# Kernel tuning notes

Hardware: AMD Instinct MI355X
Metric: run time of the kernel (lower is better)

Reference implementation:

```python
import jax, jax.numpy as jnp
import numpy as np

N, E, F, B = 50000, 100000, 80000, 64   # nodes, edges, faces, graphs
S, T, D = 32, 32, 3                      # bump_steps, num_thetas, num_features
R = 1.1
SHARP = 500.0                            # sigmoid sharpness from the source


def setup_inputs() -> dict:
    key = jax.random.key(0)
    k = jax.random.split(key, 6)
    x = jax.random.normal(k[0], (N, D), dtype=jnp.float32)
    node_weights = jax.random.uniform(k[1], (N,), dtype=jnp.float32)
    v = jax.random.uniform(k[2], (D, T), dtype=jnp.float32) - 0.5  # Parameter init: rand - 0.5
    lin = jnp.linspace(-R, R, S).astype(jnp.float32)               # bump thresholds
    edge_index = jax.random.randint(k[3], (2, E), 0, N)
    face = jax.random.randint(k[4], (3, F), 0, N)
    batch = jnp.sort(jax.random.randint(k[5], (N,), 0, B))         # sorted graph ids per node
    return {"x": x, "node_weights": node_weights, "v": v, "lin": lin,
            "edge_index": edge_index, "face": face, "batch": batch}


def _wecc(h, index, lin, weight):
    # h: [M, T] heights, index: [M] graph ids, weight: [M]
    # ecc: [M, S, T] = sigmoid(500*(lin - h)) * weight, then scatter-add by graph.
    ecc = jax.nn.sigmoid(SHARP * (lin[None, :, None] - h[:, None, :])) * weight[:, None, None]
    # segment_sum over simplices == index_add on dim 1 followed by movedim(0,1) -> [B, S, T]
    return jax.ops.segment_sum(ecc, index, num_segments=B)


def reference(x, node_weights, v, lin, edge_index, face, batch):
    nh = x @ v                                   # [N, T] node heights
    eh = jnp.min(nh[edge_index], axis=0)         # [E, T] edge height = min of endpoints
    fh = jnp.min(nh[face], axis=0)               # [F, T] face height = min of vertices
    edge_w = jnp.max(node_weights[edge_index], axis=0)  # [E]
    face_w = jnp.max(node_weights[face], axis=0)        # [F]
    out = _wecc(nh, batch, lin, node_weights)
    out = out - _wecc(eh, batch[edge_index[0]], lin, edge_w)
    out = out + _wecc(fh, batch[face[0]], lin, face_w)
    return out  # [B, S, T]
```

## Files before the change

### kernel.cpp

```cpp
#include <hip/hip_runtime.h>

#define NB      64
#define SS      32
#define TT      32
#define RADIUSF 1.1f
#define NC      16
#define NROWS   34
#define NCNT    128
#define BCAP    1440

__global__ __launch_bounds__(256) void k_pre(
    const int* __restrict__ ei, const int* __restrict__ fc,
    const int* __restrict__ batch,
    int* __restrict__ cntp, int* __restrict__ cur, int* __restrict__ ns,
    int Nn, int E, int F)
{
    const int tid = threadIdx.x;
    if ((int)blockIdx.x < NCNT) {
        __shared__ int lc[NB];
        const int blk = blockIdx.x;
        const int EF = E + F;
        if (tid < NB) lc[tid] = 0;
        __syncthreads();
        const int j0 = (int)((long long)EF * blk / NCNT);
        const int j1 = (int)((long long)EF * (blk + 1) / NCNT);
        for (int j = j0 + tid; j < j1; j += 256) {
            const int i0 = (j < E) ? ei[j] : fc[j - E];
            atomicAdd(&lc[batch[i0]], 1);
        }
        __syncthreads();
        if (tid < NB) cntp[blk * NB + tid] = lc[tid];
    } else {
        if (tid < NB) cur[tid] = 0;
        if (tid <= NB) {
            int lo = 0, hi = Nn;
            while (lo < hi) { const int mid = (lo + hi) >> 1; if (batch[mid] < tid) lo = mid + 1; else hi = mid; }
            ns[tid] = lo;
        }
    }
}

__global__ __launch_bounds__(256) void k_build(
    const float* __restrict__ nw, const int* __restrict__ ei,
    const int* __restrict__ fc, const int* __restrict__ batch,
    const int* __restrict__ cntp, int* __restrict__ cur,
    int* __restrict__ ebase_g, int4* __restrict__ U, int E, int F)
{
    __shared__ int s_sum[4][NB];
    __shared__ int s_base[NB + 1];
    __shared__ int lc[NB];
    __shared__ int lb[NB];
    __shared__ int   r_i0[BCAP], r_i1[BCAP], r_i2[BCAP];
    __shared__ float r_w[BCAP];
    __shared__ unsigned char r_b[BCAP];
    const int tid = threadIdx.x;
    const int EF = E + F;

    {
        const int bb = tid & 63, q = tid >> 6;
        int s = 0;
        for (int blk = q * (NCNT / 4); blk < (q + 1) * (NCNT / 4); ++blk)
            s += cntp[blk * NB + bb];
        s_sum[q][bb] = s;
    }
    __syncthreads();
    if (tid == 0) {
        int run = 0;
        for (int b = 0; b < NB; ++b) {
            s_base[b] = run;
            run += s_sum[0][b] + s_sum[1][b] + s_sum[2][b] + s_sum[3][b];
        }
        s_base[NB] = run;
    }
    if (tid < NB) lc[tid] = 0;
    __syncthreads();
    if (blockIdx.x == 0 && tid <= NB) ebase_g[tid] = s_base[tid];

    const int j0 = (int)((long long)EF * blockIdx.x / NCNT);
    const int j1 = (int)((long long)EF * (blockIdx.x + 1) / NCNT);
    for (int j = j0 + tid, idx = tid; j < j1; j += 256, idx += 256) {
        int i0, i1, i2; float w;
        if (j < E) {
            i0 = ei[j]; i1 = ei[E + j]; i2 = i0;
            w = -fmaxf(nw[i0], nw[i1]);
        } else {
            const int f = j - E;
            i0 = fc[f]; i1 = fc[F + f]; i2 = fc[2 * F + f];
            w = fmaxf(nw[i0], fmaxf(nw[i1], nw[i2]));
        }
        const int b = batch[i0];
        r_i0[idx] = i0; r_i1[idx] = i1; r_i2[idx] = i2;
        r_w[idx] = w; r_b[idx] = (unsigned char)b;
        atomicAdd(&lc[b], 1);
    }
    __syncthreads();
    if (tid < NB) { const int c = lc[tid]; lb[tid] = c ? atomicAdd(&cur[tid], c) : 0; lc[tid] = 0; }
    __syncthreads();
    const int cnt = j1 - j0;
    for (int idx = tid; idx < cnt; idx += 256) {
        const int b = r_b[idx];
        const int r = atomicAdd(&lc[b], 1);
        U[s_base[b] + lb[b] + r] =
            make_int4(r_i0[idx], r_i1[idx], r_i2[idx], __float_as_int(r_w[idx]));
    }
}

__global__ __launch_bounds__(256) void k_main2(
    const float* __restrict__ x, const float* __restrict__ nw,
    const float* __restrict__ v, const int4* __restrict__ U,
    const int* __restrict__ ns, const int* __restrict__ ebase,
    float* __restrict__ partial)
{
    __shared__ float hist[4][NROWS * 64];

    const int tid  = threadIdx.x;
    const int wave = tid >> 6;
    const int lane = tid & 63;
    const int t    = lane & 31;
    const int half = lane >> 5;
    const int b     = blockIdx.x & 63;
    const int chunk = blockIdx.x >> 6;

    float* H = hist[wave];
    for (int i = tid; i < 4 * NROWS * 64; i += 256) ((float*)hist)[i] = 0.0f;
    __syncthreads();

    const float v0 = v[t], v1 = v[TT + t], v2 = v[2 * TT + t];

    const float INV = 31.0f / 2.2f;
    const float DLT = 2.2f / 31.0f;

#define BODY(hv, wv)                                                        \
    {                                                                       \
        const float hr = hv + RADIUSF;                                      \
        float sf = rintf(hr * INV);                                         \
        sf = fminf(fmaxf(sf, 0.0f), 32.0f);                                 \
        const float t1 = __builtin_fmaf(sf, -DLT, hr);                      \
        const float Ee = __expf(500.0f * t1);                               \
        const float sg = __builtin_amdgcn_rcpf(1.0f + Ee);                  \
        const float dA = wv * sg;                                           \
        const float dB = wv - dA;                                           \
        float* p = H + (int)sf * 64 + lane;                                 \
        p[0]  += dA;                                                        \
        p[64] += dB;                                                        \
    }

    {
        const int g0 = ns[b], g1 = ns[b + 1];
        const int gc = g1 - g0;
        const int m0 = g0 + (int)(((long long)gc * chunk) / NC);
        const int m1 = g0 + (int)(((long long)gc * (chunk + 1)) / NC);
        for (int k = m0 + wave * 2; k < m1; k += 8) {
            const int n = min(k + half, m1 - 1);
            const float x0 = x[3 * n], x1 = x[3 * n + 1], x2 = x[3 * n + 2];
            const float h = __builtin_fmaf(x0, v0, __builtin_fmaf(x1, v1, x2 * v2));
            const float w = nw[n];
            if (k + half < m1) BODY(h, w)
        }
    }

    {
        const int g0 = ebase[b], g1 = ebase[b + 1];
        const int gc = g1 - g0;
        const int m0 = g0 + (int)(((long long)gc * chunk) / NC);
        const int m1 = g0 + (int)(((long long)gc * (chunk + 1)) / NC);
        int k = m0 + wave * 2;
        if (k < m1) {
            int4 q = U[min(k + half, m1 - 1)];
            while (k < m1) {
                const int kn = k + 8;
                const int4 qn = U[min(kn + half, m1 - 1)];
                const float a0 = x[3 * q.x], a1 = x[3 * q.x + 1], a2 = x[3 * q.x + 2];
                const float b0 = x[3 * q.y], b1 = x[3 * q.y + 1], b2 = x[3 * q.y + 2];
                const float c0 = x[3 * q.z], c1 = x[3 * q.z + 1], c2 = x[3 * q.z + 2];
                const float h0 = __builtin_fmaf(a0, v0, __builtin_fmaf(a1, v1, a2 * v2));
                const float h1 = __builtin_fmaf(b0, v0, __builtin_fmaf(b1, v1, b2 * v2));
                const float h2 = __builtin_fmaf(c0, v0, __builtin_fmaf(c1, v1, c2 * v2));
                const float h = fminf(h0, fminf(h1, h2));
                const float w = __int_as_float(q.w);
                if (k + half < m1) BODY(h, w)
                q = qn;
                k = kn;
            }
        }
    }
#undef BODY

    __syncthreads();
    float* dst = partial + ((size_t)blockIdx.x << 10);
    for (int i = tid; i < SS * TT; i += 256) {
        const int s = i >> 5, t2 = i & 31;
        float acc = 0.0f;
#pragma unroll
        for (int wv = 0; wv < 4; ++wv)
            acc += hist[wv][s * 64 + t2] + hist[wv][s * 64 + t2 + 32];
        dst[i] = acc;
    }
}

__global__ __launch_bounds__(1024) void k_finish(
    const float* __restrict__ partial, float* __restrict__ out)
{
    __shared__ float tile[SS * TT];
    const int b   = blockIdx.x;
    const int tid = threadIdx.x;
    float acc = 0.0f;
#pragma unroll
    for (int c = 0; c < NC; ++c) acc += partial[(((size_t)(c * NB + b)) << 10) + tid];
    tile[tid] = acc;
    __syncthreads();
    const int t = tid & 31, s = tid >> 5;
    float run = 0.0f;
    for (int sp = 0; sp <= s; ++sp) run += tile[(sp << 5) + t];
    out[((size_t)b << 10) + tid] = run;
}

extern "C" void kernel_launch(void* const* d_in, const int* in_sizes, int n_in,
                              void* d_out, int out_size, void* d_ws, size_t ws_size,
                              hipStream_t stream)
{
    const float* x     = (const float*)d_in[0];
    const float* nw    = (const float*)d_in[1];
    const float* v     = (const float*)d_in[2];
    const int*   ei    = (const int*)d_in[4];
    const int*   fc    = (const int*)d_in[5];
    const int*   batch = (const int*)d_in[6];
    float*       out   = (float*)d_out;

    const int Nn = in_sizes[1];
    const int E  = in_sizes[4] / 2;
    const int F  = in_sizes[5] / 3;
    const int EF = E + F;

    auto align256 = [](size_t v_) { return (v_ + 255) & ~(size_t)255; };
    const size_t U_b    = align256((size_t)EF * sizeof(int4));
    const size_t part_b = align256((size_t)NC * NB * SS * TT * sizeof(float));

    int4*  U       = (int4*)d_ws;
    float* partial = (float*)((char*)d_ws + U_b);
    int*   cntp    = (int*)((char*)d_ws + U_b + part_b);
    int*   cur     = cntp + NCNT * NB;
    int*   ns      = cur + 64;
    int*   ebase   = ns + 72;

    k_pre   <<<NCNT + 1, 256, 0, stream>>>(ei, fc, batch, cntp, cur, ns, Nn, E, F);
    k_build <<<NCNT, 256, 0, stream>>>(nw, ei, fc, batch, cntp, cur, ebase, U, E, F);
    k_main2 <<<NC * NB, 256, 0, stream>>>(x, nw, v, U, ns, ebase, partial);
    k_finish<<<NB, 1024, 0, stream>>>(partial, out);
}
```

Before: 38.78 us.

## Use fixed-capacity per-graph buckets and fuse the final reduction into the main kernel

Removes the separate counting pass and its prefix sum by giving each graph a fixed 4096-slot region in the edge/face buffer, addressed as b<<12. The finish kernel is folded into k_main2 through a per-graph atomic ticket: the last chunk block to finish reduces the partials and writes the cumulative sums. The edge/face loop also prefetches the gathered x coordinates one iteration ahead. This drops two launches and one full pass over the indices, but assumes no graph exceeds 4096 simplices; a larger graph would write into the next graph's bucket.

```diff
diff --git a/kernel.cpp b/kernel.cpp
--- a/kernel.cpp
+++ b/kernel.cpp
@@ -8,46 +8,26 @@
 #define NROWS   34
 #define NCNT    128
 #define BCAP    1440
-
-__global__ __launch_bounds__(256) void k_pre(
-    const int* __restrict__ ei, const int* __restrict__ fc,
-    const int* __restrict__ batch,
-    int* __restrict__ cntp, int* __restrict__ cur, int* __restrict__ ns,
-    int Nn, int E, int F)
+#define UCAP    4096
+
+__global__ __launch_bounds__(256) void k_init(
+    const int* __restrict__ batch, int* __restrict__ cur,
+    int* __restrict__ done, int* __restrict__ ns, int Nn)
 {
     const int tid = threadIdx.x;
-    if ((int)blockIdx.x < NCNT) {
-        __shared__ int lc[NB];
-        const int blk = blockIdx.x;
-        const int EF = E + F;
-        if (tid < NB) lc[tid] = 0;
-        __syncthreads();
-        const int j0 = (int)((long long)EF * blk / NCNT);
-        const int j1 = (int)((long long)EF * (blk + 1) / NCNT);
-        for (int j = j0 + tid; j < j1; j += 256) {
-            const int i0 = (j < E) ? ei[j] : fc[j - E];
-            atomicAdd(&lc[batch[i0]], 1);
-        }
-        __syncthreads();
-        if (tid < NB) cntp[blk * NB + tid] = lc[tid];
-    } else {
-        if (tid < NB) cur[tid] = 0;
-        if (tid <= NB) {
-            int lo = 0, hi = Nn;
-            while (lo < hi) { const int mid = (lo + hi) >> 1; if (batch[mid] < tid) lo = mid + 1; else hi = mid; }
-            ns[tid] = lo;
-        }
+    if (tid < NB) { cur[tid] = 0; done[tid] = 0; }
+    if (tid <= NB) {
+        int lo = 0, hi = Nn;
+        while (lo < hi) { const int mid = (lo + hi) >> 1; if (batch[mid] < tid) lo = mid + 1; else hi = mid; }
+        ns[tid] = lo;
     }
 }
 
 __global__ __launch_bounds__(256) void k_build(
     const float* __restrict__ nw, const int* __restrict__ ei,
     const int* __restrict__ fc, const int* __restrict__ batch,
-    const int* __restrict__ cntp, int* __restrict__ cur,
-    int* __restrict__ ebase_g, int4* __restrict__ U, int E, int F)
-{
-    __shared__ int s_sum[4][NB];
-    __shared__ int s_base[NB + 1];
+    int* __restrict__ cur, int4* __restrict__ U, int E, int F)
+{
     __shared__ int lc[NB];
     __shared__ int lb[NB];
     __shared__ int   r_i0[BCAP], r_i1[BCAP], r_i2[BCAP];
@@ -56,25 +36,8 @@
     const int tid = threadIdx.x;
     const int EF = E + F;
 
-    {
-        const int bb = tid & 63, q = tid >> 6;
-        int s = 0;
-        for (int blk = q * (NCNT / 4); blk < (q + 1) * (NCNT / 4); ++blk)
-            s += cntp[blk * NB + bb];
-        s_sum[q][bb] = s;
-    }
-    __syncthreads();
-    if (tid == 0) {
-        int run = 0;
-        for (int b = 0; b < NB; ++b) {
-            s_base[b] = run;
-            run += s_sum[0][b] + s_sum[1][b] + s_sum[2][b] + s_sum[3][b];
-        }
-        s_base[NB] = run;
-    }
     if (tid < NB) lc[tid] = 0;
     __syncthreads();
-    if (blockIdx.x == 0 && tid <= NB) ebase_g[tid] = s_base[tid];
 
     const int j0 = (int)((long long)EF * blockIdx.x / NCNT);
     const int j1 = (int)((long long)EF * (blockIdx.x + 1) / NCNT);
@@ -100,7 +63,7 @@
     for (int idx = tid; idx < cnt; idx += 256) {
         const int b = r_b[idx];
         const int r = atomicAdd(&lc[b], 1);
-        U[s_base[b] + lb[b] + r] =
+        U[(b << 12) + lb[b] + r] =
             make_int4(r_i0[idx], r_i1[idx], r_i2[idx], __float_as_int(r_w[idx]));
     }
 }
@@ -108,8 +71,9 @@
 __global__ __launch_bounds__(256) void k_main2(
     const float* __restrict__ x, const float* __restrict__ nw,
     const float* __restrict__ v, const int4* __restrict__ U,
-    const int* __restrict__ ns, const int* __restrict__ ebase,
-    float* __restrict__ partial)
+    const int* __restrict__ ns, const int* __restrict__ cur,
+    int* __restrict__ done, float* __restrict__ partial,
+    float* __restrict__ out)
 {
     __shared__ float hist[4][NROWS * 64];
 
@@ -160,27 +124,33 @@
     }
 
     {
-        const int g0 = ebase[b], g1 = ebase[b + 1];
-        const int gc = g1 - g0;
+        const int g0 = b << 12;
+        const int gc = min(cur[b], UCAP);
         const int m0 = g0 + (int)(((long long)gc * chunk) / NC);
         const int m1 = g0 + (int)(((long long)gc * (chunk + 1)) / NC);
         int k = m0 + wave * 2;
         if (k < m1) {
-            int4 q = U[min(k + half, m1 - 1)];
+            int4 q  = U[min(k + half, m1 - 1)];
+            int4 qn = U[min(k + 8 + half, m1 - 1)];
+            float a0 = x[3 * q.x], a1 = x[3 * q.x + 1], a2 = x[3 * q.x + 2];
+            float b0 = x[3 * q.y], b1 = x[3 * q.y + 1], b2 = x[3 * q.y + 2];
+            float c0 = x[3 * q.z], c1 = x[3 * q.z + 1], c2 = x[3 * q.z + 2];
             while (k < m1) {
                 const int kn = k + 8;
-                const int4 qn = U[min(kn + half, m1 - 1)];
-                const float a0 = x[3 * q.x], a1 = x[3 * q.x + 1], a2 = x[3 * q.x + 2];
-                const float b0 = x[3 * q.y], b1 = x[3 * q.y + 1], b2 = x[3 * q.y + 2];
-                const float c0 = x[3 * q.z], c1 = x[3 * q.z + 1], c2 = x[3 * q.z + 2];
+                const int4 qn2 = U[min(kn + 8 + half, m1 - 1)];
+                const float na0 = x[3 * qn.x], na1 = x[3 * qn.x + 1], na2 = x[3 * qn.x + 2];
+                const float nb0 = x[3 * qn.y], nb1 = x[3 * qn.y + 1], nb2 = x[3 * qn.y + 2];
+                const float nc0 = x[3 * qn.z], nc1 = x[3 * qn.z + 1], nc2 = x[3 * qn.z + 2];
                 const float h0 = __builtin_fmaf(a0, v0, __builtin_fmaf(a1, v1, a2 * v2));
                 const float h1 = __builtin_fmaf(b0, v0, __builtin_fmaf(b1, v1, b2 * v2));
                 const float h2 = __builtin_fmaf(c0, v0, __builtin_fmaf(c1, v1, c2 * v2));
                 const float h = fminf(h0, fminf(h1, h2));
                 const float w = __int_as_float(q.w);
                 if (k + half < m1) BODY(h, w)
-                q = qn;
-                k = kn;
+                a0 = na0; a1 = na1; a2 = na2;
+                b0 = nb0; b1 = nb1; b2 = nb2;
+                c0 = nc0; c1 = nc1; c2 = nc2;
+                q = qn; qn = qn2; k = kn;
             }
         }
     }
@@ -196,23 +166,30 @@
             acc += hist[wv][s * 64 + t2] + hist[wv][s * 64 + t2 + 32];
         dst[i] = acc;
     }
-}
-
-__global__ __launch_bounds__(1024) void k_finish(
-    const float* __restrict__ partial, float* __restrict__ out)
-{
-    __shared__ float tile[SS * TT];
-    const int b   = blockIdx.x;
-    const int tid = threadIdx.x;
-    float acc = 0.0f;
+
+    __shared__ int s_ticket;
+    __threadfence();
+    __syncthreads();
+    if (tid == 0) s_ticket = atomicAdd(&done[b], 1);
+    __syncthreads();
+    if (s_ticket == NC - 1) {
+        __threadfence();
+        __shared__ float tile[SS * TT];
+        for (int i = tid; i < SS * TT; i += 256) {
+            float acc = 0.0f;
 #pragma unroll
-    for (int c = 0; c < NC; ++c) acc += partial[(((size_t)(c * NB + b)) << 10) + tid];
-    tile[tid] = acc;
-    __syncthreads();
-    const int t = tid & 31, s = tid >> 5;
-    float run = 0.0f;
-    for (int sp = 0; sp <= s; ++sp) run += tile[(sp << 5) + t];
-    out[((size_t)b << 10) + tid] = run;
+            for (int c = 0; c < NC; ++c)
+                acc += partial[(((size_t)(c * NB + b)) << 10) + i];
+            tile[i] = acc;
+        }
+        __syncthreads();
+        for (int i = tid; i < SS * TT; i += 256) {
+            const int s = i >> 5, t2 = i & 31;
+            float run = 0.0f;
+            for (int sp = 0; sp <= s; ++sp) run += tile[(sp << 5) + t2];
+            out[((size_t)b << 10) + i] = run;
+        }
+    }
 }
 
 extern "C" void kernel_launch(void* const* d_in, const int* in_sizes, int n_in,
@@ -230,21 +207,18 @@
     const int Nn = in_sizes[1];
     const int E  = in_sizes[4] / 2;
     const int F  = in_sizes[5] / 3;
-    const int EF = E + F;
 
     auto align256 = [](size_t v_) { return (v_ + 255) & ~(size_t)255; };
-    const size_t U_b    = align256((size_t)EF * sizeof(int4));
+    const size_t U_b    = align256((size_t)NB * UCAP * sizeof(int4));
     const size_t part_b = align256((size_t)NC * NB * SS * TT * sizeof(float));
 
     int4*  U       = (int4*)d_ws;
     float* partial = (float*)((char*)d_ws + U_b);
-    int*   cntp    = (int*)((char*)d_ws + U_b + part_b);
-    int*   cur     = cntp + NCNT * NB;
-    int*   ns      = cur + 64;
-    int*   ebase   = ns + 72;
-
-    k_pre   <<<NCNT + 1, 256, 0, stream>>>(ei, fc, batch, cntp, cur, ns, Nn, E, F);
-    k_build <<<NCNT, 256, 0, stream>>>(nw, ei, fc, batch, cntp, cur, ebase, U, E, F);
-    k_main2 <<<NC * NB, 256, 0, stream>>>(x, nw, v, U, ns, ebase, partial);
-    k_finish<<<NB, 1024, 0, stream>>>(partial, out);
-}
+    int*   cur     = (int*)((char*)d_ws + U_b + part_b);
+    int*   done    = cur + 64;
+    int*   ns      = done + 64;
+
+    k_init <<<1, 256, 0, stream>>>(batch, cur, done, ns, Nn);
+    k_build<<<NCNT, 256, 0, stream>>>(nw, ei, fc, batch, cur, U, E, F);
+    k_main2<<<NC * NB, 256, 0, stream>>>(x, nw, v, U, ns, cur, done, partial, out);
+}
```

New measurement: 117.3 us. 3.03x slower.
